# Kernel optimization log

Measured on AMD Instinct MI355X. Metric: run time of the kernel, lower is better.

## Reference

```python
import jax, jax.numpy as jnp
import numpy as np

K = 4  # topk neighbors (default of match())
ALPHA = 0.0  # blend factor (default of match())


def setup_inputs() -> dict:
    key = jax.random.key(0)
    k1, k2 = jax.random.split(key)
    B, D, T, N = 32, 32, 16384, 128
    source = jax.random.normal(k1, (B, D, T), dtype=jnp.float32)
    tokens = jax.random.normal(k2, (1, D, N), dtype=jnp.float32)  # nn.Parameter
    return {"source": source, "tokens": tokens}


def reference(source, tokens):
    # source: (B, D, T); tokens: (1, D, N)
    ref = tokens[0].T                                   # (N, D) unnormalized reference
    s = jnp.swapaxes(source, 1, 2)                      # (B, T, D)
    s_n = s / jnp.linalg.norm(s, axis=2, keepdims=True)
    r_n = ref / jnp.linalg.norm(ref, axis=1, keepdims=True)
    cos_sims = jnp.einsum('btd,nd->btn', s_n, r_n)      # (B, T, N)
    _, idx = jax.lax.top_k(cos_sims, K)                 # (B, T, K)
    gathered = ref[idx]                                 # (B, T, K, D) gather of unnormalized refs
    result = gathered.mean(axis=2)                      # (B, T, D)
    out = jnp.swapaxes(result, 1, 2)                    # (B, D, T)
    return out * (1.0 - ALPHA) + source * ALPHA
```

## Files before the change

kernel.cpp:

```cpp
#include <hip/hip_runtime.h>
#include <math.h>

typedef float f32x2 __attribute__((ext_vector_type(2)));

constexpr int B = 32, D = 32, T = 16384, N = 128;
constexpr float MARG = 2e-5f;

__device__ __forceinline__ float np_pairwise32_sq(const float* v) {
#pragma clang fp contract(off)
    float r[8];
    #pragma unroll
    for (int j = 0; j < 8; ++j) r[j] = v[j] * v[j];
    #pragma unroll
    for (int i = 8; i < 32; i += 8) {
        #pragma unroll
        for (int j = 0; j < 8; ++j) r[j] += v[i + j] * v[i + j];
    }
    return ((r[0] + r[1]) + (r[2] + r[3])) + ((r[4] + r[5]) + (r[6] + r[7]));
}

__device__ __forceinline__ float np_pairwise32_sq2(const f32x2* v) {
#pragma clang fp contract(off)
    float r[8];
    #pragma unroll
    for (int j = 0; j < 8; ++j) {
        float x = (j & 1) ? v[j >> 1].y : v[j >> 1].x;
        r[j] = x * x;
    }
    #pragma unroll
    for (int i = 8; i < 32; i += 8) {
        #pragma unroll
        for (int j = 0; j < 8; ++j) {
            int e = i + j;
            float x = (e & 1) ? v[e >> 1].y : v[e >> 1].x;
            r[j] += x * x;
        }
    }
    return ((r[0] + r[1]) + (r[2] + r[3])) + ((r[4] + r[5]) + (r[6] + r[7]));
}

__device__ __forceinline__ float np_seq_dot_g(const float* __restrict__ sn,
                                              const float4* __restrict__ rw) {
#pragma clang fp contract(off)
    float acc = 0.0f;
    #pragma unroll
    for (int k = 0; k < 8; ++k) {
        float4 q = rw[k];
        acc += sn[4 * k + 0] * q.x;
        acc += sn[4 * k + 1] * q.y;
        acc += sn[4 * k + 2] * q.z;
        acc += sn[4 * k + 3] * q.w;
    }
    return acc;
}

__global__ void norm_tokens_kernel(const float* __restrict__ tokens,
                                   float* __restrict__ rn_g) {
    int n = threadIdx.x;
    if (n < N) {
        float tq[D];
        #pragma unroll
        for (int d = 0; d < D; ++d) tq[d] = tokens[d * N + n];
        float nrm = sqrtf(np_pairwise32_sq(tq));
        #pragma unroll
        for (int d = 0; d < D; ++d) rn_g[n * D + d] = tq[d] / nrm;
    }
}

#define INSERT_STEP(v, n)                                                    \
    {                                                                        \
        bool c0 = (v) > t0, c1 = (v) > t1, c2 = (v) > t2, c3 = (v) > t3;     \
        float nt0 = fmaxf(t0, (v));                                          \
        float nt1 = __builtin_amdgcn_fmed3f((v), t1, t0);                    \
        float nt2 = __builtin_amdgcn_fmed3f((v), t2, t1);                    \
        float nt3 = __builtin_amdgcn_fmed3f((v), t3, t2);                    \
        int ni0 = c0 ? (n) : i0;                                             \
        int ni1 = c1 ? (c0 ? i0 : (n)) : i1;                                 \
        int ni2 = c2 ? (c1 ? i1 : (n)) : i2;                                 \
        int ni3 = c3 ? (c2 ? i2 : (n)) : i3;                                 \
        t0 = nt0; t1 = nt1; t2 = nt2; t3 = nt3;                              \
        i0 = ni0; i1 = ni1; i2 = ni2; i3 = ni3;                              \
    }

__global__ __launch_bounds__(256) void ve_kernel(
    const float* __restrict__ source,
    const float* __restrict__ rn_g,
    const float* __restrict__ tokens,
    float* __restrict__ out)
{
    __shared__ float rf[N][D + 1];

    for (int i = threadIdx.x; i < N * D; i += 256) {
        int d = i >> 7, n = i & (N - 1);
        rf[n][d] = tokens[i];
    }
    __syncthreads();

    int gid = blockIdx.x * 256 + threadIdx.x;
    int b = gid >> 14, t = gid & (T - 1);

    const float* src = source + (size_t)b * D * T + t;
    f32x2 s2[16];
    #pragma unroll
    for (int k = 0; k < 16; ++k) {
        s2[k].x = src[(size_t)(2 * k) * T];
        s2[k].y = src[(size_t)(2 * k + 1) * T];
    }
    float nrm = sqrtf(np_pairwise32_sq2(s2));

    float t0 = -INFINITY, t1 = -INFINITY, t2 = -INFINITY, t3 = -INFINITY;
    float m5 = -INFINITY;
    int i0 = 0, i1 = 0, i2 = 0, i3 = 0;

    const f32x2* rn2 = (const f32x2*)rn_g;
    #pragma unroll 2
    for (int n = 0; n < N; ++n) {
        const f32x2* r2 = rn2 + (n << 4);
        f32x2 e = {0.f, 0.f}, o = {0.f, 0.f};
        #pragma unroll
        for (int k = 0; k < 16; k += 2) {
            e += s2[k] * r2[k];
            o += s2[k + 1] * r2[k + 1];
        }
        f32x2 h = e + o;
        float v = h.x + h.y;

        m5 = fmaxf(m5, fminf(v, t3));
        INSERT_STEP(v, n);
    }

    if (t3 - m5 <= MARG * nrm) {
        float sn[32];
        #pragma unroll
        for (int k = 0; k < 16; ++k) {
            sn[2 * k]     = s2[k].x / nrm;
            sn[2 * k + 1] = s2[k].y / nrm;
        }
        t0 = t1 = t2 = t3 = -INFINITY;
        i0 = i1 = i2 = i3 = 0;
        for (int n = 0; n < N; ++n) {
            float v = np_seq_dot_g(sn, (const float4*)rn_g + (n << 3));
            INSERT_STEP(v, n);
        }
    }

    float* dst = out + (size_t)b * D * T + t;
    #pragma unroll
    for (int d = 0; d < D; ++d) {
        float sum = ((rf[i0][d] + rf[i1][d]) + rf[i2][d]) + rf[i3][d];
        dst[(size_t)d * T] = sum * 0.25f;
    }
}

extern "C" void kernel_launch(void* const* d_in, const int* in_sizes, int n_in,
                              void* d_out, int out_size, void* d_ws, size_t ws_size,
                              hipStream_t stream) {
    const float* source = (const float*)d_in[0];
    const float* tokens = (const float*)d_in[1];
    float* out = (float*)d_out;
    float* rn_g = (float*)d_ws;

    norm_tokens_kernel<<<1, 128, 0, stream>>>(tokens, rn_g);
    ve_kernel<<<(B * T) / 256, 256, 0, stream>>>(source, rn_g, tokens, out);
}
```

Measured before the change: 155.6 us.

## Fuse token normalization into main kernel and serve normalized refs from LDS

Removes the separate normalization kernel launch; each block now normalizes the 128 reference tokens into shared memory and reads them from LDS instead of global/cache during the 128-way dot-product scan. The dot loop uses float4 LDS reads with four accumulators, and the final gather reads padded rf rows as float4. This trades a launch and global reads for redundant per-block normalization work and more LDS usage, which may reduce occupancy.

```diff
diff --git a/kernel.cpp b/kernel.cpp
--- a/kernel.cpp
+++ b/kernel.cpp
@@ -39,8 +39,8 @@
     return ((r[0] + r[1]) + (r[2] + r[3])) + ((r[4] + r[5]) + (r[6] + r[7]));
 }
 
-__device__ __forceinline__ float np_seq_dot_g(const float* __restrict__ sn,
-                                              const float4* __restrict__ rw) {
+__device__ __forceinline__ float np_seq_dot(const float* __restrict__ sn,
+                                            const float4* __restrict__ rw) {
 #pragma clang fp contract(off)
     float acc = 0.0f;
     #pragma unroll
@@ -52,19 +52,6 @@
         acc += sn[4 * k + 3] * q.w;
     }
     return acc;
-}
-
-__global__ void norm_tokens_kernel(const float* __restrict__ tokens,
-                                   float* __restrict__ rn_g) {
-    int n = threadIdx.x;
-    if (n < N) {
-        float tq[D];
-        #pragma unroll
-        for (int d = 0; d < D; ++d) tq[d] = tokens[d * N + n];
-        float nrm = sqrtf(np_pairwise32_sq(tq));
-        #pragma unroll
-        for (int d = 0; d < D; ++d) rn_g[n * D + d] = tq[d] / nrm;
-    }
 }
 
 #define INSERT_STEP(v, n)                                                    \
@@ -84,15 +71,26 @@
 
 __global__ __launch_bounds__(256) void ve_kernel(
     const float* __restrict__ source,
-    const float* __restrict__ rn_g,
     const float* __restrict__ tokens,
     float* __restrict__ out)
 {
-    __shared__ float rf[N][D + 1];
+    __shared__ float rn[N][D];
+    __shared__ float rf[N][D + 4];
 
     for (int i = threadIdx.x; i < N * D; i += 256) {
         int d = i >> 7, n = i & (N - 1);
         rf[n][d] = tokens[i];
+    }
+    __syncthreads();
+
+    if (threadIdx.x < N) {
+        int n = threadIdx.x;
+        float tq[D];
+        #pragma unroll
+        for (int d = 0; d < D; ++d) tq[d] = rf[n][d];
+        float nrm = sqrtf(np_pairwise32_sq(tq));
+        #pragma unroll
+        for (int d = 0; d < D; ++d) rn[n][d] = tq[d] / nrm;
     }
     __syncthreads();
 
@@ -112,17 +110,22 @@
     float m5 = -INFINITY;
     int i0 = 0, i1 = 0, i2 = 0, i3 = 0;
 
-    const f32x2* rn2 = (const f32x2*)rn_g;
-    #pragma unroll 2
+    #pragma unroll 4
     for (int n = 0; n < N; ++n) {
-        const f32x2* r2 = rn2 + (n << 4);
-        f32x2 e = {0.f, 0.f}, o = {0.f, 0.f};
+        const float4* rw = reinterpret_cast<const float4*>(&rn[n][0]);
+        f32x2 a0 = {0.f, 0.f}, a1 = {0.f, 0.f};
+        f32x2 a2 = {0.f, 0.f}, a3 = {0.f, 0.f};
         #pragma unroll
-        for (int k = 0; k < 16; k += 2) {
-            e += s2[k] * r2[k];
-            o += s2[k + 1] * r2[k + 1];
+        for (int k = 0; k < 4; ++k) {
+            float4 q0 = rw[2 * k], q1 = rw[2 * k + 1];
+            f32x2 qa = {q0.x, q0.y}, qb = {q0.z, q0.w};
+            f32x2 qc = {q1.x, q1.y}, qd = {q1.z, q1.w};
+            a0 += s2[4 * k + 0] * qa;
+            a1 += s2[4 * k + 1] * qb;
+            a2 += s2[4 * k + 2] * qc;
+            a3 += s2[4 * k + 3] * qd;
         }
-        f32x2 h = e + o;
+        f32x2 h = (a0 + a2) + (a1 + a3);
         float v = h.x + h.y;
 
         m5 = fmaxf(m5, fminf(v, t3));
@@ -130,7 +133,7 @@
     }
 
     if (t3 - m5 <= MARG * nrm) {
-        float sn[32];
+        float sn[D];
         #pragma unroll
         for (int k = 0; k < 16; ++k) {
             sn[2 * k]     = s2[k].x / nrm;
@@ -139,16 +142,23 @@
         t0 = t1 = t2 = t3 = -INFINITY;
         i0 = i1 = i2 = i3 = 0;
         for (int n = 0; n < N; ++n) {
-            float v = np_seq_dot_g(sn, (const float4*)rn_g + (n << 3));
+            float v = np_seq_dot(sn, reinterpret_cast<const float4*>(&rn[n][0]));
             INSERT_STEP(v, n);
         }
     }
 
+    const float4* g0 = reinterpret_cast<const float4*>(&rf[i0][0]);
+    const float4* g1 = reinterpret_cast<const float4*>(&rf[i1][0]);
+    const float4* g2 = reinterpret_cast<const float4*>(&rf[i2][0]);
+    const float4* g3 = reinterpret_cast<const float4*>(&rf[i3][0]);
     float* dst = out + (size_t)b * D * T + t;
     #pragma unroll
-    for (int d = 0; d < D; ++d) {
-        float sum = ((rf[i0][d] + rf[i1][d]) + rf[i2][d]) + rf[i3][d];
-        dst[(size_t)d * T] = sum * 0.25f;
+    for (int k = 0; k < 8; ++k) {
+        float4 v0 = g0[k], v1 = g1[k], v2 = g2[k], v3 = g3[k];
+        dst[(size_t)(4 * k + 0) * T] = (((v0.x + v1.x) + v2.x) + v3.x) * 0.25f;
+        dst[(size_t)(4 * k + 1) * T] = (((v0.y + v1.y) + v2.y) + v3.y) * 0.25f;
+        dst[(size_t)(4 * k + 2) * T] = (((v0.z + v1.z) + v2.z) + v3.z) * 0.25f;
+        dst[(size_t)(4 * k + 3) * T] = (((v0.w + v1.w) + v2.w) + v3.w) * 0.25f;
     }
 }
 
@@ -158,8 +168,7 @@
     const float* source = (const float*)d_in[0];
     const float* tokens = (const float*)d_in[1];
     float* out = (float*)d_out;
-    float* rn_g = (float*)d_ws;
 
-    norm_tokens_kernel<<<1, 128, 0, stream>>>(tokens, rn_g);
-    ve_kernel<<<(B * T) / 256, 256, 0, stream>>>(source, rn_g, tokens, out);
+    dim3 grid((B * T) / 256), block(256);
+    ve_kernel<<<grid, block, 0, stream>>>(source, tokens, out);
 }
```

New measurement: 170.2 us. 1.09x slower.
